# Performance work log

Measured on AMD Instinct MI355X. Metric: run time of the kernel, lower is better.

Reference implementation:

```python
import jax, jax.numpy as jnp
import numpy as np

EPS = 1e-6       # eps from __init__
STEPSIZE = 1.0   # stepsize from __init__
DELTA = 0.1      # delta from __init__


def setup_inputs() -> dict:
    key = jax.random.key(0)
    k1, k2, k3 = jax.random.split(key, 3)
    N, L, H, E, M = 2, 2048, 8, 64, 64
    return {
        "queries": jax.random.normal(k1, (N, L, H, E), dtype=jnp.float32),
        "keys": jax.random.normal(k2, (N, L, H, E), dtype=jnp.float32),
        "values": jax.random.normal(k3, (N, L, H, M), dtype=jnp.float32),
        "key_lengths_mask": jnp.ones((N, L), dtype=jnp.float32),
    }


def reference(queries, keys, values, key_lengths_mask):
    # elu feature map: elu(x) + 1
    Q = jax.nn.elu(queries) + 1.0                                   # [N,L,H,E]
    K = (jax.nn.elu(keys) + 1.0) * key_lengths_mask[:, :, None, None]
    N, L, H, E = Q.shape

    # normalizer Z_t = 1 / (q_t . sum_{s<=t} k_s + eps)
    Z = 1.0 / (jnp.einsum('nlhe,nlhe->nlh', Q, jnp.cumsum(K, axis=1)) + EPS)

    # per-step outer products k_s v_s^T  (original materializes this einsum)
    KV = jnp.einsum('nlhe,nlhm->nlhem', K, values)                  # [N,L,H,E,M]

    # causal_dot_product: out_t = q_t . cumsum_s(KV)_t
    out = jnp.einsum('nlhe,nlhem->nlhm', Q, jnp.cumsum(KV, axis=1)) * Z[..., None]

    # momentum coefficients mu_j from Frobenius norms over (E,M)
    diff_norm = jnp.sqrt(jnp.sum((KV[:, 1:] - KV[:, :-1]) ** 2, axis=(3, 4)))  # [N,L-1,H]
    base_norm = jnp.sqrt(jnp.sum(KV[:, :-1] ** 2, axis=(3, 4)))
    mu = jnp.clip((1.0 - jnp.sqrt(diff_norm / base_norm)) ** 2, 0.0, 1.0 - DELTA)

    # momentum weights: a_{L-1}=1, a_j = 1 + mu_j * a_{j+1} (backward recurrence).
    # This equals both momentum_weight (cumprod-sum form) and momentum_weight_old
    # (explicit reverse loop) in the original, so Kn == Kw.
    def step(a, mu_t):
        a_new = 1.0 + mu_t * a
        return a_new, a_new

    _, a_seq = jax.lax.scan(step, jnp.ones((N, H), Q.dtype),
                            jnp.moveaxis(mu, 1, 0), reverse=True)   # [L-1,N,H]
    momentum_weight = jnp.concatenate(
        [jnp.moveaxis(a_seq, 0, 1), jnp.ones((N, 1, H), Q.dtype)], axis=1)  # [N,L,H]
    Kn = K * momentum_weight[..., None] * STEPSIZE                  # [N,L,H,E]

    return out, Kn
```

## Files before the change

### kernel.cpp

```cpp
#include <hip/hip_runtime.h>

#define N_ 2
#define L_ 2048
#define H_ 8
#define NH_ 16
#define C_ 64
#define NC_ 32
#define EPS_ 1e-6f
#define DELTA_ 0.1f

#define CHSZ 4160
#define ST_SHORTS (NH_*NC_*CHSZ)
#define KV_SHORTS (NH_*L_*64)

typedef short s8v __attribute__((ext_vector_type(8)));
typedef short s4v __attribute__((ext_vector_type(4)));
typedef float f4v __attribute__((ext_vector_type(4)));

__device__ __forceinline__ float elup1(float x){ return x>0.f ? x+1.f : __expf(x); }
__device__ __forceinline__ short f2b(float x){
  unsigned u = __float_as_uint(x);
  return (short)((u + 0x7FFFu + ((u>>16)&1u)) >> 16);
}
__device__ __forceinline__ float b2f(short s){
  return __uint_as_float(((unsigned)(unsigned short)s) << 16);
}

__global__ __launch_bounds__(256) void kA(const float* __restrict__ keys,
    const float* __restrict__ values, const float* __restrict__ mask,
    unsigned short* __restrict__ st, short* __restrict__ ktil,
    short* __restrict__ vtilT, float* __restrict__ mu)
{
  const int bid = blockIdx.x, c = bid & (NC_-1), nh = bid >> 5;
  const int n = nh >> 3, h = nh & 7, tid = threadIdx.x;
  const int lane = tid & 63, w = tid >> 6, r = lane & 15, g = lane >> 4;

  __shared__ __attribute__((aligned(16))) short Ktb[64][72];
  __shared__ __attribute__((aligned(16))) short Vtb[80][72];
  __shared__ float prt[6][4][64];

  #pragma unroll
  for (int i = 0; i < 4; ++i) {
    const int idx4 = tid + 256*i;
    const int t = idx4 >> 4, e4 = (idx4 & 15) << 2;
    const int l = c*C_ + t;
    const size_t b = (((size_t)n*L_ + l)*H_ + h)*64 + e4;
    const float m0 = mask[n*L_ + l];
    const f4v kx = *(const f4v*)&keys[b];
    const f4v vx = *(const f4v*)&values[b];
    s4v kb4;
    #pragma unroll
    for (int j = 0; j < 4; ++j) kb4[j] = f2b(elup1(kx[j]) * m0);
    *(s4v*)&ktil[((size_t)nh*L_ + l)*64 + e4] = kb4;
    #pragma unroll
    for (int j = 0; j < 4; ++j) { Ktb[e4+j][t] = kb4[j]; Vtb[e4+j][t] = f2b(vx[j]); }
  }
  if (tid < 64) Vtb[64][tid] = (short)0x3F80;
  __syncthreads();

  #pragma unroll
  for (int i = 0; i < 2; ++i) {
    const int idx8 = tid + 256*i;
    const int m = idx8 >> 3, t8 = (idx8 & 7) << 3;
    *(s8v*)&vtilT[((size_t)bid*64 + m)*64 + t8] = *(const s8v*)&Vtb[m][t8];
  }

  {
    f4v acc[5];
    #pragma unroll
    for (int j = 0; j < 5; ++j) acc[j] = (f4v)(0.f);
    #pragma unroll
    for (int k2 = 0; k2 < 2; ++k2) {
      const s8v a = *(const s8v*)&Ktb[w*16 + r][k2*32 + g*8];
      #pragma unroll
      for (int mj = 0; mj < 5; ++mj) {
        const s8v bb = *(const s8v*)&Vtb[mj*16 + r][k2*32 + g*8];
        acc[mj] = __builtin_amdgcn_mfma_f32_16x16x32_bf16(a, bb, acc[mj], 0, 0, 0);
      }
    }
    unsigned short* sp = st + (size_t)bid*CHSZ;
    #pragma unroll
    for (int mj = 0; mj < 5; ++mj) {
      const int m = mj*16 + r;
      if (m <= 64) {
        s4v pk;
        #pragma unroll
        for (int j = 0; j < 4; ++j) pk[j] = f2b(acc[mj][j]);
        *(s4v*)&sp[(size_t)m*64 + w*16 + g*4] = pk;
      }
    }
  }

  {
    const int t = lane, eq = w;
    const int l = c*C_ + t;
    const int l1 = (l+1 < L_) ? l+1 : l;
    const size_t b0 = (((size_t)n*L_ + l )*H_ + h)*64 + eq*16;
    const size_t b1 = (((size_t)n*L_ + l1)*H_ + h)*64 + eq*16;
    const float m0 = mask[n*L_ + l], m1 = mask[n*L_ + l1];
    float kk0=0.f,kk1=0.f,knn=0.f,vv0=0.f,vv1=0.f,vnn=0.f;
    #pragma unroll
    for (int j = 0; j < 16; j += 4) {
      const f4v ka = *(const f4v*)&keys[b0+j];
      const f4v kc = *(const f4v*)&keys[b1+j];
      const f4v va = *(const f4v*)&values[b0+j];
      const f4v vc = *(const f4v*)&values[b1+j];
      #pragma unroll
      for (int jj = 0; jj < 4; ++jj) {
        const float k0 = elup1(ka[jj])*m0, k1 = elup1(kc[jj])*m1;
        kk0 += k0*k0; kk1 += k1*k1; knn += k0*k1;
        const float v0 = va[jj], v1 = vc[jj];
        vv0 += v0*v0; vv1 += v1*v1; vnn += v0*v1;
      }
    }
    prt[0][eq][t]=kk0; prt[1][eq][t]=kk1; prt[2][eq][t]=knn;
    prt[3][eq][t]=vv0; prt[4][eq][t]=vv1; prt[5][eq][t]=vnn;
  }
  __syncthreads();
  if (tid < 64) {
    float s[6];
    #pragma unroll
    for (int q2 = 0; q2 < 6; ++q2)
      s[q2] = prt[q2][0][tid]+prt[q2][1][tid]+prt[q2][2][tid]+prt[q2][3][tid];
    const int j = c*C_ + tid;
    float mval = 0.f;
    if (j < L_-1) {
      const float base2 = s[0]*s[3];
      float diff2 = s[1]*s[4] - 2.f*s[2]*s[5] + base2;
      diff2 = fmaxf(diff2, 0.f);
      if (base2 > 0.f) {
        const float r4 = sqrtf(sqrtf(diff2/base2));
        const float om = 1.f - r4;
        mval = fminf(om*om, 1.f - DELTA_);
      } else {
        mval = 1.f - DELTA_;
      }
    }
    mu[(size_t)nh*L_ + j] = mval;
  }
}

__global__ __launch_bounds__(256) void kBC(unsigned short* __restrict__ st,
    const float* __restrict__ mu, float* __restrict__ aw)
{
  const int bx = blockIdx.x, tid = threadIdx.x;
  if (bx < 260) {
    const int id = bx*256 + tid;
    const int nh2 = id / CHSZ;
    const int elem = id - nh2*CHSZ;
    unsigned short* base = st + (size_t)nh2*NC_*CHSZ + elem;
    unsigned short rr[NC_];
    #pragma unroll
    for (int c2 = 0; c2 < NC_; ++c2) rr[c2] = base[(size_t)c2*CHSZ];
    float acc = 0.f;
    #pragma unroll
    for (int c2 = 0; c2 < NC_; ++c2) {
      const float v = b2f((short)rr[c2]);
      base[(size_t)c2*CHSZ] = (unsigned short)f2b(acc);
      acc += v;
    }
    return;
  }
  const int nh2 = bx - 260;
  const float* mup = mu + (size_t)nh2*L_;
  float* awp = aw + (size_t)nh2*L_;
  __shared__ float Psc[256], Qsc[256];
  float lm[8];
  #pragma unroll
  for (int i = 0; i < 8; ++i) lm[i] = mup[tid*8 + i];
  float p = 1.f, q = 0.f;
  #pragma unroll
  for (int i = 7; i >= 0; --i) { q = lm[i]*q + 1.f; p *= lm[i]; }
  Psc[tid] = p; Qsc[tid] = q;
  __syncthreads();
  for (int d = 1; d < 256; d <<= 1) {
    float pr = 1.f, qr = 0.f;
    const bool has = (tid + d) < 256;
    if (has) { pr = Psc[tid+d]; qr = Qsc[tid+d]; }
    __syncthreads();
    if (has) { const float np = p*pr, nq = p*qr + q; p = np; q = nq; Psc[tid] = p; Qsc[tid] = q; }
    __syncthreads();
  }
  float x = (tid == 255) ? 1.f : Psc[tid+1] + Qsc[tid+1];
  #pragma unroll
  for (int i = 7; i >= 0; --i) { x = lm[i]*x + 1.f; awp[tid*8+i] = x; }
}

__global__ __launch_bounds__(256) void kD(const float* __restrict__ queries,
    const unsigned short* __restrict__ st, const short* __restrict__ ktil,
    const short* __restrict__ vtilT, const float* __restrict__ aw,
    float* __restrict__ out, float* __restrict__ kn)
{
  const int bid = blockIdx.x, c = bid & (NC_-1), nh = bid >> 5;
  const int n = nh >> 3, h = nh & 7, tid = threadIdx.x;
  const int lane = tid & 63, w = tid >> 6, r = lane & 15, g = lane >> 4;

  __shared__ __attribute__((aligned(16))) short Qb[64][72];
  __shared__ __attribute__((aligned(16))) short Kb[64][72];
  __shared__ __attribute__((aligned(16))) short Pb[64][72];
  __shared__ float al[64];

  const unsigned short* sp = st + (size_t)bid*CHSZ;
  const short* vp = vtilT + (size_t)bid*64*64;

  s8v sfrag[2][4], srow64[2];
  const s8v zero8 = (s8v)(0);
  #pragma unroll
  for (int k2 = 0; k2 < 2; ++k2) {
    #pragma unroll
    for (int mj = 0; mj < 4; ++mj)
      sfrag[k2][mj] = *(const s8v*)&sp[(size_t)(mj*16 + r)*64 + k2*32 + g*8];
    srow64[k2] = (r == 0) ? *(const s8v*)&sp[(size_t)64*64 + k2*32 + g*8] : zero8;
  }

  #pragma unroll
  for (int i = 0; i < 4; ++i) {
    const int idx4 = tid + 256*i;
    const int t = idx4 >> 4, e4 = (idx4 & 15) << 2;
    const int l = c*C_ + t;
    const f4v qx = __builtin_nontemporal_load(
        (const f4v*)&queries[(((size_t)n*L_ + l)*H_ + h)*64 + e4]);
    s4v qb4;
    #pragma unroll
    for (int j = 0; j < 4; ++j) qb4[j] = f2b(elup1(qx[j]));
    *(s4v*)&Qb[t][e4] = qb4;
  }
  for (int idx = tid; idx < 512; idx += 256) {
    const int t = idx >> 3, e8 = (idx & 7) << 3;
    *(s8v*)&Kb[t][e8] = *(const s8v*)&ktil[((size_t)nh*L_ + c*C_ + t)*64 + e8];
  }
  if (tid < 64) al[tid] = aw[(size_t)nh*L_ + c*C_ + tid];
  __syncthreads();

  {
    f4v pacc[4];
    #pragma unroll
    for (int tj = 0; tj < 4; ++tj) pacc[tj] = (f4v)(0.f);
    #pragma unroll
    for (int k2 = 0; k2 < 2; ++k2) {
      const s8v a = *(const s8v*)&Kb[w*16 + r][k2*32 + g*8];
      #pragma unroll
      for (int tj = 0; tj < 4; ++tj) {
        const s8v bb = *(const s8v*)&Qb[tj*16 + r][k2*32 + g*8];
        pacc[tj] = __builtin_amdgcn_mfma_f32_16x16x32_bf16(a, bb, pacc[tj], 0, 0, 0);
      }
    }
    #pragma unroll
    for (int tj = 0; tj < 4; ++tj) {
      const int t = tj*16 + r;
      s4v pk;
      #pragma unroll
      for (int j = 0; j < 4; ++j) {
        const int s2 = w*16 + g*4 + j;
        pk[j] = (s2 <= t) ? f2b(pacc[tj][j]) : (short)0;
      }
      *(s4v*)&Pb[t][w*16 + g*4] = pk;
    }
  }

  s8v vfrag[2][4], vones;
  #pragma unroll
  for (int k2 = 0; k2 < 2; ++k2)
    #pragma unroll
    for (int mj = 0; mj < 4; ++mj)
      vfrag[k2][mj] = *(const s8v*)&vp[(size_t)(mj*16 + r)*64 + k2*32 + g*8];
  {
    s8v o;
    #pragma unroll
    for (int j = 0; j < 8; ++j) o[j] = (short)0x3F80;
    vones = (r == 0) ? o : zero8;
  }
  __syncthreads();

  f4v oacc[5];
  #pragma unroll
  for (int j = 0; j < 5; ++j) oacc[j] = (f4v)(0.f);
  #pragma unroll
  for (int k2 = 0; k2 < 4; ++k2) {
    const s8v a = (k2 < 2) ? *(const s8v*)&Qb[w*16 + r][k2*32 + g*8]
                           : *(const s8v*)&Pb[w*16 + r][(k2-2)*32 + g*8];
    #pragma unroll
    for (int mj = 0; mj < 5; ++mj) {
      const s8v bb = (k2 < 2) ? ((mj < 4) ? sfrag[k2][mj] : srow64[k2])
                              : ((mj < 4) ? vfrag[k2-2][mj] : vones);
      oacc[mj] = __builtin_amdgcn_mfma_f32_16x16x32_bf16(a, bb, oacc[mj], 0, 0, 0);
    }
  }

  {
    float z[4];
    #pragma unroll
    for (int j = 0; j < 4; ++j) {
      const float dj = __shfl(oacc[4][j], g << 4);
      z[j] = 1.f / (dj + EPS_);
    }
    float* obase = out + (((size_t)n*L_ + c*C_ + w*16)*H_ + h)*64;
    #pragma unroll
    for (int mj = 0; mj < 4; ++mj)
      #pragma unroll
      for (int j = 0; j < 4; ++j)
        __builtin_nontemporal_store(oacc[mj][j] * z[j],
            &obase[(size_t)(g*4 + j)*H_*64 + mj*16 + r]);
  }
  #pragma unroll
  for (int i = 0; i < 4; ++i) {
    const int idx4 = tid + 256*i;
    const int t = idx4 >> 4, e4 = (idx4 & 15) << 2, l = c*C_ + t;
    const float a2 = al[t];
    const s4v kb4 = *(const s4v*)&Kb[t][e4];
    f4v o;
    #pragma unroll
    for (int j = 0; j < 4; ++j) o[j] = b2f(kb4[j]) * a2;
    __builtin_nontemporal_store(o, (f4v*)&kn[(((size_t)n*L_ + l)*H_ + h)*64 + e4]);
  }
}

extern "C" void kernel_launch(void* const* d_in, const int* in_sizes, int n_in,
                              void* d_out, int out_size, void* d_ws, size_t ws_size,
                              hipStream_t stream) {
  (void)in_sizes; (void)n_in; (void)out_size; (void)ws_size;
  const float* queries = (const float*)d_in[0];
  const float* keys    = (const float*)d_in[1];
  const float* values  = (const float*)d_in[2];
  const float* mask    = (const float*)d_in[3];
  float* out = (float*)d_out;
  float* kn  = out + (size_t)N_*L_*H_*64;

  unsigned short* st = (unsigned short*)d_ws;
  short* ktil = (short*)(st + ST_SHORTS);
  short* vtilT = ktil + KV_SHORTS;
  float* mu = (float*)(vtilT + KV_SHORTS);
  float* aw = mu + NH_*L_;

  hipLaunchKernelGGL(kA,  dim3(NH_*NC_), dim3(256), 0, stream,
                     keys, values, mask, st, ktil, vtilT, mu);
  hipLaunchKernelGGL(kBC, dim3(276),     dim3(256), 0, stream, st, mu, aw);
  hipLaunchKernelGGL(kD,  dim3(NH_*NC_), dim3(256), 0, stream,
                     queries, st, ktil, vtilT, aw, out, kn);
}
```

Baseline: 29.45 us.

## Double block size to 512 threads, split MFMA work and stage outputs via LDS

kA and kD now launch 512-thread blocks. In kA, half the waves run the KV-state MFMA while the other half compute the mu norm statistics concurrently. In kD, waves are split across output column groups (3+2 tiles including the normalizer column), fully masked causal P tiles are skipped, and the output is staged through an LDS union buffer so global stores are coalesced float4 rows. This aims to raise occupancy and overlap within the memory-bound 512-block grid, at the cost of extra barriers, more LDS and uneven per-wave MFMA work.

```diff
diff --git a/kernel.cpp b/kernel.cpp
--- a/kernel.cpp
+++ b/kernel.cpp
@@ -26,22 +26,21 @@
   return __uint_as_float(((unsigned)(unsigned short)s) << 16);
 }
 
-__global__ __launch_bounds__(256) void kA(const float* __restrict__ keys,
+__global__ __launch_bounds__(512) void kA(const float* __restrict__ keys,
     const float* __restrict__ values, const float* __restrict__ mask,
     unsigned short* __restrict__ st, short* __restrict__ ktil,
     short* __restrict__ vtilT, float* __restrict__ mu)
 {
   const int bid = blockIdx.x, c = bid & (NC_-1), nh = bid >> 5;
   const int n = nh >> 3, h = nh & 7, tid = threadIdx.x;
-  const int lane = tid & 63, w = tid >> 6, r = lane & 15, g = lane >> 4;
 
   __shared__ __attribute__((aligned(16))) short Ktb[64][72];
   __shared__ __attribute__((aligned(16))) short Vtb[80][72];
   __shared__ float prt[6][4][64];
 
   #pragma unroll
-  for (int i = 0; i < 4; ++i) {
-    const int idx4 = tid + 256*i;
+  for (int i = 0; i < 2; ++i) {
+    const int idx4 = tid + 512*i;
     const int t = idx4 >> 4, e4 = (idx4 & 15) << 2;
     const int l = c*C_ + t;
     const size_t b = (((size_t)n*L_ + l)*H_ + h)*64 + e4;
@@ -58,14 +57,13 @@
   if (tid < 64) Vtb[64][tid] = (short)0x3F80;
   __syncthreads();
 
-  #pragma unroll
-  for (int i = 0; i < 2; ++i) {
-    const int idx8 = tid + 256*i;
-    const int m = idx8 >> 3, t8 = (idx8 & 7) << 3;
+  {
+    const int m = tid >> 3, t8 = (tid & 7) << 3;
     *(s8v*)&vtilT[((size_t)bid*64 + m)*64 + t8] = *(const s8v*)&Vtb[m][t8];
   }
 
-  {
+  if (tid < 256) {
+    const int lane = tid & 63, w = tid >> 6, r = lane & 15, g = lane >> 4;
     f4v acc[5];
     #pragma unroll
     for (int j = 0; j < 5; ++j) acc[j] = (f4v)(0.f);
@@ -89,10 +87,9 @@
         *(s4v*)&sp[(size_t)m*64 + w*16 + g*4] = pk;
       }
     }
-  }
-
-  {
-    const int t = lane, eq = w;
+  } else {
+    const int tid2 = tid - 256;
+    const int t = tid2 & 63, eq = tid2 >> 6;
     const int l = c*C_ + t;
     const int l1 = (l+1 < L_) ? l+1 : l;
     const size_t b0 = (((size_t)n*L_ + l )*H_ + h)*64 + eq*16;
@@ -186,7 +183,7 @@
   for (int i = 7; i >= 0; --i) { x = lm[i]*x + 1.f; awp[tid*8+i] = x; }
 }
 
-__global__ __launch_bounds__(256) void kD(const float* __restrict__ queries,
+__global__ __launch_bounds__(512) void kD(const float* __restrict__ queries,
     const unsigned short* __restrict__ st, const short* __restrict__ ktil,
     const short* __restrict__ vtilT, const float* __restrict__ aw,
     float* __restrict__ out, float* __restrict__ kn)
@@ -194,28 +191,38 @@
   const int bid = blockIdx.x, c = bid & (NC_-1), nh = bid >> 5;
   const int n = nh >> 3, h = nh & 7, tid = threadIdx.x;
   const int lane = tid & 63, w = tid >> 6, r = lane & 15, g = lane >> 4;
+  const int tt = w & 3, mg = w >> 2;
 
   __shared__ __attribute__((aligned(16))) short Qb[64][72];
   __shared__ __attribute__((aligned(16))) short Kb[64][72];
-  __shared__ __attribute__((aligned(16))) short Pb[64][72];
-  __shared__ float al[64];
+  __shared__ __attribute__((aligned(16))) union {
+    short Pb[64][72];
+    float outf[64][68];
+  } U;
+  __shared__ float Zl[64], al[64];
 
   const unsigned short* sp = st + (size_t)bid*CHSZ;
-  const short* vp = vtilT + (size_t)bid*64*64;
-
-  s8v sfrag[2][4], srow64[2];
+  const short* vp = vtilT + (size_t)bid*4096;
   const s8v zero8 = (s8v)(0);
+
+  s8v sfrag[2][3], srow64[2];
   #pragma unroll
   for (int k2 = 0; k2 < 2; ++k2) {
-    #pragma unroll
-    for (int mj = 0; mj < 4; ++mj)
-      sfrag[k2][mj] = *(const s8v*)&sp[(size_t)(mj*16 + r)*64 + k2*32 + g*8];
-    srow64[k2] = (r == 0) ? *(const s8v*)&sp[(size_t)64*64 + k2*32 + g*8] : zero8;
-  }
-
-  #pragma unroll
-  for (int i = 0; i < 4; ++i) {
-    const int idx4 = tid + 256*i;
+    if (mg == 0) {
+      #pragma unroll
+      for (int mi = 0; mi < 3; ++mi)
+        sfrag[k2][mi] = *(const s8v*)&sp[(size_t)(mi*16 + r)*64 + k2*32 + g*8];
+      srow64[k2] = zero8;
+    } else {
+      sfrag[k2][0] = *(const s8v*)&sp[(size_t)(48 + r)*64 + k2*32 + g*8];
+      srow64[k2] = (r == 0) ? *(const s8v*)&sp[(size_t)64*64 + k2*32 + g*8] : zero8;
+      sfrag[k2][1] = zero8; sfrag[k2][2] = zero8;
+    }
+  }
+
+  #pragma unroll
+  for (int i = 0; i < 2; ++i) {
+    const int idx4 = tid + 512*i;
     const int t = idx4 >> 4, e4 = (idx4 & 15) << 2;
     const int l = c*C_ + t;
     const f4v qx = __builtin_nontemporal_load(
@@ -225,86 +232,109 @@
     for (int j = 0; j < 4; ++j) qb4[j] = f2b(elup1(qx[j]));
     *(s4v*)&Qb[t][e4] = qb4;
   }
-  for (int idx = tid; idx < 512; idx += 256) {
-    const int t = idx >> 3, e8 = (idx & 7) << 3;
+  {
+    const int t = tid >> 3, e8 = (tid & 7) << 3;
     *(s8v*)&Kb[t][e8] = *(const s8v*)&ktil[((size_t)nh*L_ + c*C_ + t)*64 + e8];
   }
   if (tid < 64) al[tid] = aw[(size_t)nh*L_ + c*C_ + tid];
   __syncthreads();
 
   {
-    f4v pacc[4];
-    #pragma unroll
-    for (int tj = 0; tj < 4; ++tj) pacc[tj] = (f4v)(0.f);
-    #pragma unroll
-    for (int k2 = 0; k2 < 2; ++k2) {
-      const s8v a = *(const s8v*)&Kb[w*16 + r][k2*32 + g*8];
-      #pragma unroll
-      for (int tj = 0; tj < 4; ++tj) {
-        const s8v bb = *(const s8v*)&Qb[tj*16 + r][k2*32 + g*8];
-        pacc[tj] = __builtin_amdgcn_mfma_f32_16x16x32_bf16(a, bb, pacc[tj], 0, 0, 0);
-      }
-    }
-    #pragma unroll
-    for (int tj = 0; tj < 4; ++tj) {
-      const int t = tj*16 + r;
+    const int ss = tt, th = mg;
+    const bool live = (ss*16) <= (th*32 + 31);
+    f4v pacc[2];
+    pacc[0] = (f4v)(0.f); pacc[1] = (f4v)(0.f);
+    if (live) {
+      #pragma unroll
+      for (int k2 = 0; k2 < 2; ++k2) {
+        const s8v a = *(const s8v*)&Kb[ss*16 + r][k2*32 + g*8];
+        #pragma unroll
+        for (int tj2 = 0; tj2 < 2; ++tj2) {
+          const s8v bb = *(const s8v*)&Qb[(th*2 + tj2)*16 + r][k2*32 + g*8];
+          pacc[tj2] = __builtin_amdgcn_mfma_f32_16x16x32_bf16(a, bb, pacc[tj2], 0, 0, 0);
+        }
+      }
+    }
+    #pragma unroll
+    for (int tj2 = 0; tj2 < 2; ++tj2) {
+      const int t = (th*2 + tj2)*16 + r;
       s4v pk;
       #pragma unroll
       for (int j = 0; j < 4; ++j) {
-        const int s2 = w*16 + g*4 + j;
-        pk[j] = (s2 <= t) ? f2b(pacc[tj][j]) : (short)0;
-      }
-      *(s4v*)&Pb[t][w*16 + g*4] = pk;
-    }
-  }
-
-  s8v vfrag[2][4], vones;
-  #pragma unroll
-  for (int k2 = 0; k2 < 2; ++k2)
-    #pragma unroll
-    for (int mj = 0; mj < 4; ++mj)
-      vfrag[k2][mj] = *(const s8v*)&vp[(size_t)(mj*16 + r)*64 + k2*32 + g*8];
+        const int s2 = ss*16 + g*4 + j;
+        pk[j] = (live && s2 <= t) ? f2b(pacc[tj2][j]) : (short)0;
+      }
+      *(s4v*)&U.Pb[t][ss*16 + g*4] = pk;
+    }
+  }
+
+  s8v vfrag[2][3], vones;
+  #pragma unroll
+  for (int k2 = 0; k2 < 2; ++k2) {
+    if (mg == 0) {
+      #pragma unroll
+      for (int mi = 0; mi < 3; ++mi)
+        vfrag[k2][mi] = *(const s8v*)&vp[(size_t)(mi*16 + r)*64 + k2*32 + g*8];
+    } else {
+      vfrag[k2][0] = *(const s8v*)&vp[(size_t)(48 + r)*64 + k2*32 + g*8];
+      vfrag[k2][1] = zero8; vfrag[k2][2] = zero8;
+    }
+  }
   {
     s8v o;
     #pragma unroll
     for (int j = 0; j < 8; ++j) o[j] = (short)0x3F80;
-    vones = (r == 0) ? o : zero8;
-  }
-  __syncthreads();
-
-  f4v oacc[5];
-  #pragma unroll
-  for (int j = 0; j < 5; ++j) oacc[j] = (f4v)(0.f);
+    vones = (r == 0 && mg == 1) ? o : zero8;
+  }
+  __syncthreads();
+
+  const int nmj = (mg == 0) ? 3 : 2;
+  f4v oacc[3];
+  #pragma unroll
+  for (int j = 0; j < 3; ++j) oacc[j] = (f4v)(0.f);
   #pragma unroll
   for (int k2 = 0; k2 < 4; ++k2) {
-    const s8v a = (k2 < 2) ? *(const s8v*)&Qb[w*16 + r][k2*32 + g*8]
-                           : *(const s8v*)&Pb[w*16 + r][(k2-2)*32 + g*8];
-    #pragma unroll
-    for (int mj = 0; mj < 5; ++mj) {
-      const s8v bb = (k2 < 2) ? ((mj < 4) ? sfrag[k2][mj] : srow64[k2])
-                              : ((mj < 4) ? vfrag[k2-2][mj] : vones);
-      oacc[mj] = __builtin_amdgcn_mfma_f32_16x16x32_bf16(a, bb, oacc[mj], 0, 0, 0);
-    }
-  }
-
-  {
-    float z[4];
-    #pragma unroll
-    for (int j = 0; j < 4; ++j) {
-      const float dj = __shfl(oacc[4][j], g << 4);
-      z[j] = 1.f / (dj + EPS_);
-    }
-    float* obase = out + (((size_t)n*L_ + c*C_ + w*16)*H_ + h)*64;
-    #pragma unroll
-    for (int mj = 0; mj < 4; ++mj)
+    const s8v a = (k2 < 2) ? *(const s8v*)&Qb[tt*16 + r][k2*32 + g*8]
+                           : *(const s8v*)&U.Pb[tt*16 + r][(k2-2)*32 + g*8];
+    #pragma unroll
+    for (int mi = 0; mi < 3; ++mi) {
+      if (mi < nmj) {
+        s8v bb;
+        if (k2 < 2) bb = (mg == 1 && mi == 1) ? srow64[k2] : sfrag[k2][mi];
+        else        bb = (mg == 1 && mi == 1) ? vones      : vfrag[k2-2][mi];
+        oacc[mi] = __builtin_amdgcn_mfma_f32_16x16x32_bf16(a, bb, oacc[mi], 0, 0, 0);
+      }
+    }
+  }
+  __syncthreads();
+
+  if (mg == 1 && r == 0) {
+    #pragma unroll
+    for (int j = 0; j < 4; ++j) Zl[tt*16 + g*4 + j] = 1.f / (oacc[1][j] + EPS_);
+  }
+  #pragma unroll
+  for (int mi = 0; mi < 3; ++mi) {
+    const int mjg = mg*3 + mi;
+    if (mi < nmj && mjg < 4) {
       #pragma unroll
       for (int j = 0; j < 4; ++j)
-        __builtin_nontemporal_store(oacc[mj][j] * z[j],
-            &obase[(size_t)(g*4 + j)*H_*64 + mj*16 + r]);
-  }
-  #pragma unroll
-  for (int i = 0; i < 4; ++i) {
-    const int idx4 = tid + 256*i;
+        U.outf[tt*16 + g*4 + j][mjg*16 + r] = oacc[mi][j];
+    }
+  }
+  __syncthreads();
+
+  #pragma unroll
+  for (int i = 0; i < 2; ++i) {
+    const int idx4 = tid + 512*i;
+    const int t = idx4 >> 4, m4 = (idx4 & 15) << 2, l = c*C_ + t;
+    f4v v = *(const f4v*)&U.outf[t][m4];
+    const float z = Zl[t];
+    v[0] *= z; v[1] *= z; v[2] *= z; v[3] *= z;
+    __builtin_nontemporal_store(v, (f4v*)&out[(((size_t)n*L_ + l)*H_ + h)*64 + m4]);
+  }
+  #pragma unroll
+  for (int i = 0; i < 2; ++i) {
+    const int idx4 = tid + 512*i;
     const int t = idx4 >> 4, e4 = (idx4 & 15) << 2, l = c*C_ + t;
     const float a2 = al[t];
     const s4v kb4 = *(const s4v*)&Kb[t][e4];
@@ -332,9 +362,9 @@
   float* mu = (float*)(vtilT + KV_SHORTS);
   float* aw = mu + NH_*L_;
 
-  hipLaunchKernelGGL(kA,  dim3(NH_*NC_), dim3(256), 0, stream,
+  hipLaunchKernelGGL(kA,  dim3(NH_*NC_), dim3(512), 0, stream,
                      keys, values, mask, st, ktil, vtilT, mu);
   hipLaunchKernelGGL(kBC, dim3(276),     dim3(256), 0, stream, st, mu, aw);
-  hipLaunchKernelGGL(kD,  dim3(NH_*NC_), dim3(256), 0, stream,
+  hipLaunchKernelGGL(kD,  dim3(NH_*NC_), dim3(512), 0, stream,
                      queries, st, ktil, vtilT, aw, out, kn);
 }
```

After: 26.79 us (median of 2 runs). 1.1x faster.
